# Kernel optimization log

Measured on AMD Instinct MI355X. Metric: run time of the kernel, lower is better.

The kernel has to match this reference:

```python
import jax, jax.numpy as jnp
import numpy as np

N_TOKENS = 16384
IN_FEATURES = 1024
OUT_FEATURES = 1024
BH = 32  # block rows (out dim)
BW = 32  # block cols (in dim)
N_BLOCKS = 256  # density 0.25 * (1024*1024/(32*32))


def setup_inputs() -> dict:
    key = jax.random.key(0)
    k1, k2, k3, k4 = jax.random.split(key, 4)
    x = jax.random.normal(k1, (N_TOKENS, IN_FEATURES), dtype=jnp.float32)
    weight_data = jax.random.normal(k2, (N_BLOCKS, BH, BW), dtype=jnp.float32)
    bias = jnp.zeros((OUT_FEATURES,), dtype=jnp.float32)
    block_row = jax.random.randint(k3, (N_BLOCKS,), 0, OUT_FEATURES // BH, dtype=jnp.int32)
    block_col = jax.random.randint(k4, (N_BLOCKS,), 0, IN_FEATURES // BW, dtype=jnp.int32)
    return {"x": x, "weight_data": weight_data, "bias": bias,
            "block_row": block_row, "block_col": block_col}


def reference(x, weight_data, bias, block_row, block_col):
    # Block-sparse linear: y = x @ W^T + bias, with W[out, in] stored as
    # N_BLOCKS dense (BH, BW) blocks at (block_row, block_col) block coords.
    N = x.shape[0]
    B, bh, bw = weight_data.shape
    n_row_blocks = bias.shape[0] // bh
    x3 = x.reshape(N, -1, bw)           # [N, in/bw, bw]
    xb = x3[:, block_col, :]            # gather input block-columns: [N, B, bw]
    # per-block partial output rows: data[b] @ x_colblock -> [N, B, bh]
    partial = jnp.einsum('nbw,bow->nbo', xb, weight_data)
    y3 = jnp.zeros((N, n_row_blocks, bh), dtype=x.dtype).at[:, block_row, :].add(partial)
    return y3.reshape(N, -1) + bias
```

## Files before the change

kernel.cpp:

```cpp
#include <hip/hip_runtime.h>

#define N_TOKENS 16384
#define IN_F 1024
#define OUT_F 1024
#define NB 256
#define BH 32
#define BW 32
#define NRB 32
#define T_TILE 32
#define NW 8
#define XS_STRIDE 1040
#define SCHED_ALLOC 304
#define WF_SLOT_SHORTS 1024
#define FLUSH_BIT (1 << 10)

#define WS_WF_BYTES   (SCHED_ALLOC * WF_SLOT_SHORTS * 2)
#define WS_SCHED_OFF  WS_WF_BYTES
#define WS_POS_OFF    (WS_SCHED_OFF + SCHED_ALLOC * 4)
#define WS_WSTART_OFF (WS_POS_OFF + NB * 4)

typedef short short8 __attribute__((ext_vector_type(8)));
typedef float float4v __attribute__((ext_vector_type(4)));

__device__ __forceinline__ short f2bf(float f) {
    unsigned u = __builtin_bit_cast(unsigned, f);
    u += 0x7fffu + ((u >> 16) & 1u);
    return (short)(u >> 16);
}

__global__ void prep_sched_kernel(const int* __restrict__ brow, const int* __restrict__ bcol,
                                  int* __restrict__ sched, int* __restrict__ pos_of,
                                  int* __restrict__ wstart, short* __restrict__ wf)
{
    __shared__ int cnt[NRB], start[NRB], cur[NRB];
    const int tid = threadIdx.x;
    if (tid < NRB) { cnt[tid] = 0; cur[tid] = 0; }
    __syncthreads();
    const int r = brow[tid];
    const int c = bcol[tid];
    atomicAdd(&cnt[r], 1);
    __syncthreads();
    if (tid < NRB) {
        const int w = tid & 7;
        int s = 0;
        for (int w2 = 0; w2 < w; ++w2) {
            int t = 0;
            for (int rr = w2; rr < NRB; rr += NW) t += (cnt[rr] ? cnt[rr] : 1);
            s += (t + 1) & ~1;
        }
        for (int rr = w; rr < tid; rr += NW) s += (cnt[rr] ? cnt[rr] : 1);
        start[tid] = s;
    }
    if (tid >= 64 && tid < 64 + NW + 1) {
        const int w = tid - 64;
        int s = 0;
        for (int w2 = 0; w2 < w; ++w2) {
            int t = 0;
            for (int rr = w2; rr < NRB; rr += NW) t += (cnt[rr] ? cnt[rr] : 1);
            s += (t + 1) & ~1;
        }
        wstart[w] = s;
    }
    if (tid >= 96 && tid < 96 + NW) {
        const int w = tid - 96;
        int base = 0;
        for (int w2 = 0; w2 < w; ++w2) {
            int t = 0;
            for (int rr = w2; rr < NRB; rr += NW) t += (cnt[rr] ? cnt[rr] : 1);
            base += (t + 1) & ~1;
        }
        int t = 0;
        for (int rr = w; rr < NRB; rr += NW) t += (cnt[rr] ? cnt[rr] : 1);
        if (t & 1) sched[base + t] = 0;
    }
    if (tid >= 128 && tid < 136) {
        int tot = 0;
        for (int w2 = 0; w2 < NW; ++w2) {
            int t = 0;
            for (int rr = w2; rr < NRB; rr += NW) t += (cnt[rr] ? cnt[rr] : 1);
            tot += (t + 1) & ~1;
        }
        sched[tot + (tid - 128)] = 0;
    }
    __syncthreads();
    const int slot = atomicAdd(&cur[r], 1);
    const int pos = start[r] + slot;
    sched[pos] = c | (r << 5) | ((slot == cnt[r] - 1) ? FLUSH_BIT : 0);
    pos_of[tid] = pos;
    if (tid < NRB && cnt[tid] == 0) {
        sched[start[tid]] = (tid << 5) | FLUSH_BIT;
        int4 z = {0, 0, 0, 0};
        int4* dst = (int4*)(wf + (size_t)start[tid] * WF_SLOT_SHORTS);
        for (int q = 0; q < WF_SLOT_SHORTS / 8; ++q) dst[q] = z;
    }
}

__global__ void prep_w_kernel(const float* __restrict__ wd, const int* __restrict__ pos_of,
                              short* __restrict__ wf)
{
    const int g = blockIdx.x * blockDim.x + threadIdx.x;
    const int lane = g & 63;
    const int oh = (g >> 6) & 1;
    const int b = g >> 7;
    const int l16 = lane & 15, quad = lane >> 4;
    const int pos = pos_of[b];
    const float* src = wd + (size_t)b * (BH * BW) + (oh * 16 + l16) * BW + quad * 8;
    const float4 w0 = *(const float4*)src;
    const float4 w1 = *(const float4*)(src + 4);
    short8 o;
    o[0] = f2bf(w0.x); o[1] = f2bf(w0.y); o[2] = f2bf(w0.z); o[3] = f2bf(w0.w);
    o[4] = f2bf(w1.x); o[5] = f2bf(w1.y); o[6] = f2bf(w1.z); o[7] = f2bf(w1.w);
    *(short8*)(wf + (size_t)pos * WF_SLOT_SHORTS + oh * 512 + lane * 8) = o;
}

__global__ __launch_bounds__(512, 4) void spmm_main_kernel(
    const float* __restrict__ x, const float* __restrict__ bias,
    const short* __restrict__ wf, const int* __restrict__ sched_g,
    const int* __restrict__ wstart_g, float* __restrict__ out)
{
    __shared__ short xs[T_TILE * XS_STRIDE];
    __shared__ int ssched[SCHED_ALLOC];
    __shared__ int swstart[NW + 1];

    const int tid = threadIdx.x;
    const int n0 = blockIdx.x * T_TILE;

    {
        const int tr = tid >> 7;
        const int tc = tid & 127;
        const float* xp = x + (size_t)(n0 + tr) * IN_F + tc * 8;
        short* sp = xs + tr * XS_STRIDE + tc * 8;
#pragma unroll
        for (int it = 0; it < T_TILE / 4; ++it) {
            const float4 a = *(const float4*)xp;
            const float4 b = *(const float4*)(xp + 4);
            short8 s;
            s[0] = f2bf(a.x); s[1] = f2bf(a.y); s[2] = f2bf(a.z); s[3] = f2bf(a.w);
            s[4] = f2bf(b.x); s[5] = f2bf(b.y); s[6] = f2bf(b.z); s[7] = f2bf(b.w);
            *(short8*)sp = s;
            xp += 4 * IN_F;
            sp += 4 * XS_STRIDE;
        }
    }
    if (tid < SCHED_ALLOC) ssched[tid] = sched_g[tid];
    if (tid < NW + 1) swstart[tid] = wstart_g[tid];
    __syncthreads();

    const int lane = tid & 63;
    const int wave = tid >> 6;
    const int l16 = lane & 15, quad = lane >> 4;

    const int s = swstart[wave];
    const int e = swstart[wave + 1];

    const short* x0 = xs + l16 * XS_STRIDE + quad * 8;
    const short* x1 = x0 + 16 * XS_STRIDE;
    const short* wfl = wf + lane * 8;

    int e0 = ssched[s], e1 = ssched[s + 1];
    int e2 = ssched[s + 2], e3 = ssched[s + 3];
    short8 cwA0 = *(const short8*)(wfl + (size_t)s * WF_SLOT_SHORTS);
    short8 cwB0 = *(const short8*)(wfl + (size_t)s * WF_SLOT_SHORTS + 512);
    short8 cwA1 = *(const short8*)(wfl + (size_t)(s + 1) * WF_SLOT_SHORTS);
    short8 cwB1 = *(const short8*)(wfl + (size_t)(s + 1) * WF_SLOT_SHORTS + 512);
    short8 nwA0 = *(const short8*)(wfl + (size_t)(s + 2) * WF_SLOT_SHORTS);
    short8 nwB0 = *(const short8*)(wfl + (size_t)(s + 2) * WF_SLOT_SHORTS + 512);
    short8 nwA1 = *(const short8*)(wfl + (size_t)(s + 3) * WF_SLOT_SHORTS);
    short8 nwB1 = *(const short8*)(wfl + (size_t)(s + 3) * WF_SLOT_SHORTS + 512);
    short8 a0t0 = *(const short8*)(x0 + (e0 & 31) * BW);
    short8 a0t1 = *(const short8*)(x1 + (e0 & 31) * BW);
    short8 a1t0 = *(const short8*)(x0 + (e1 & 31) * BW);
    short8 a1t1 = *(const short8*)(x1 + (e1 & 31) * BW);

    int rn = wave;
    float bv0 = bias[rn * BH + l16];
    float bv1 = bias[rn * BH + 16 + l16];

    float4v accA = {0.f, 0.f, 0.f, 0.f};
    float4v accB = {0.f, 0.f, 0.f, 0.f};
    float4v accC = {0.f, 0.f, 0.f, 0.f};
    float4v accD = {0.f, 0.f, 0.f, 0.f};

    auto flush = [&](int ev) {
        if (ev & FLUSH_BIT) {
            const int rr = (ev >> 5) & 31;
            const int ob = rr * BH + l16;
            float* op0 = out + (size_t)(n0 + quad * 4) * OUT_F + ob;
            float* op1 = op0 + (size_t)16 * OUT_F;
#pragma unroll
            for (int g = 0; g < 4; ++g) {
                op0[g * OUT_F]      = accA[g] + bv0;
                op0[g * OUT_F + 16] = accB[g] + bv1;
                op1[g * OUT_F]      = accC[g] + bv0;
                op1[g * OUT_F + 16] = accD[g] + bv1;
            }
            accA = (float4v){0.f, 0.f, 0.f, 0.f};
            accB = (float4v){0.f, 0.f, 0.f, 0.f};
            accC = (float4v){0.f, 0.f, 0.f, 0.f};
            accD = (float4v){0.f, 0.f, 0.f, 0.f};
            rn = (rn + NW) & 31;
            bv0 = bias[rn * BH + l16];
            bv1 = bias[rn * BH + 16 + l16];
        }
    };

    for (int k = s; k < e; k += 2) {
        const int e4 = ssched[k + 4];
        const int e5 = ssched[k + 5];
        const short8 fwA0 = *(const short8*)(wfl + (size_t)(k + 4) * WF_SLOT_SHORTS);
        const short8 fwB0 = *(const short8*)(wfl + (size_t)(k + 4) * WF_SLOT_SHORTS + 512);
        const short8 fwA1 = *(const short8*)(wfl + (size_t)(k + 5) * WF_SLOT_SHORTS);
        const short8 fwB1 = *(const short8*)(wfl + (size_t)(k + 5) * WF_SLOT_SHORTS + 512);
        const short8 na0t0 = *(const short8*)(x0 + (e2 & 31) * BW);
        const short8 na0t1 = *(const short8*)(x1 + (e2 & 31) * BW);
        const short8 na1t0 = *(const short8*)(x0 + (e3 & 31) * BW);
        const short8 na1t1 = *(const short8*)(x1 + (e3 & 31) * BW);

        accA = __builtin_amdgcn_mfma_f32_16x16x32_bf16(a0t0, cwA0, accA, 0, 0, 0);
        accB = __builtin_amdgcn_mfma_f32_16x16x32_bf16(a0t0, cwB0, accB, 0, 0, 0);
        accC = __builtin_amdgcn_mfma_f32_16x16x32_bf16(a0t1, cwA0, accC, 0, 0, 0);
        accD = __builtin_amdgcn_mfma_f32_16x16x32_bf16(a0t1, cwB0, accD, 0, 0, 0);
        flush(e0);
        accA = __builtin_amdgcn_mfma_f32_16x16x32_bf16(a1t0, cwA1, accA, 0, 0, 0);
        accB = __builtin_amdgcn_mfma_f32_16x16x32_bf16(a1t0, cwB1, accB, 0, 0, 0);
        accC = __builtin_amdgcn_mfma_f32_16x16x32_bf16(a1t1, cwA1, accC, 0, 0, 0);
        accD = __builtin_amdgcn_mfma_f32_16x16x32_bf16(a1t1, cwB1, accD, 0, 0, 0);
        flush(e1);

        e0 = e2; e1 = e3; e2 = e4; e3 = e5;
        a0t0 = na0t0; a0t1 = na0t1; a1t0 = na1t0; a1t1 = na1t1;
        cwA0 = nwA0; cwB0 = nwB0; cwA1 = nwA1; cwB1 = nwB1;
        nwA0 = fwA0; nwB0 = fwB0; nwA1 = fwA1; nwB1 = fwB1;
    }
}

extern "C" void kernel_launch(void* const* d_in, const int* in_sizes, int n_in,
                              void* d_out, int out_size, void* d_ws, size_t ws_size,
                              hipStream_t stream) {
    const float* x    = (const float*)d_in[0];
    const float* wd   = (const float*)d_in[1];
    const float* bias = (const float*)d_in[2];
    const int* brow   = (const int*)d_in[3];
    const int* bcol   = (const int*)d_in[4];
    float* out = (float*)d_out;

    char* ws = (char*)d_ws;
    short* wf   = (short*)ws;
    int* sched  = (int*)(ws + WS_SCHED_OFF);
    int* pos_of = (int*)(ws + WS_POS_OFF);
    int* wstart = (int*)(ws + WS_WSTART_OFF);

    prep_sched_kernel<<<1, 256, 0, stream>>>(brow, bcol, sched, pos_of, wstart, wf);
    prep_w_kernel<<<NB * 128 / 256, 256, 0, stream>>>(wd, pos_of, wf);
    spmm_main_kernel<<<N_TOKENS / T_TILE, 512, 0, stream>>>(x, bias, wf, sched, wstart, out);
}
```

Before: 134.8 us.

## Halve token tile, balance row-blocks across waves by load, cache bias in LDS

```diff
diff --git a/kernel.cpp b/kernel.cpp
--- a/kernel.cpp
+++ b/kernel.cpp
@@ -7,7 +7,7 @@
 #define BH 32
 #define BW 32
 #define NRB 32
-#define T_TILE 32
+#define T_TILE 16
 #define NW 8
 #define XS_STRIDE 1040
 #define SCHED_ALLOC 304
@@ -33,6 +33,8 @@
                                   int* __restrict__ wstart, short* __restrict__ wf)
 {
     __shared__ int cnt[NRB], start[NRB], cur[NRB];
+    __shared__ int eff[NRB], rnk[NRB], wv[NRB], off[NRB];
+    __shared__ int wtot[NW], pw[NW + 1];
     const int tid = threadIdx.x;
     if (tid < NRB) { cnt[tid] = 0; cur[tid] = 0; }
     __syncthreads();
@@ -40,48 +42,47 @@
     const int c = bcol[tid];
     atomicAdd(&cnt[r], 1);
     __syncthreads();
+    if (tid < NRB) eff[tid] = cnt[tid] ? cnt[tid] : 1;
+    __syncthreads();
     if (tid < NRB) {
-        const int w = tid & 7;
-        int s = 0;
-        for (int w2 = 0; w2 < w; ++w2) {
-            int t = 0;
-            for (int rr = w2; rr < NRB; rr += NW) t += (cnt[rr] ? cnt[rr] : 1);
-            s += (t + 1) & ~1;
+        const int e_ = eff[tid];
+        int rk = 0;
+        for (int j = 0; j < NRB; ++j) {
+            const int ej = eff[j];
+            if (ej > e_ || (ej == e_ && j < tid)) ++rk;
         }
-        for (int rr = w; rr < tid; rr += NW) s += (cnt[rr] ? cnt[rr] : 1);
-        start[tid] = s;
-    }
-    if (tid >= 64 && tid < 64 + NW + 1) {
-        const int w = tid - 64;
-        int s = 0;
-        for (int w2 = 0; w2 < w; ++w2) {
-            int t = 0;
-            for (int rr = w2; rr < NRB; rr += NW) t += (cnt[rr] ? cnt[rr] : 1);
-            s += (t + 1) & ~1;
-        }
-        wstart[w] = s;
-    }
-    if (tid >= 96 && tid < 96 + NW) {
-        const int w = tid - 96;
-        int base = 0;
-        for (int w2 = 0; w2 < w; ++w2) {
-            int t = 0;
-            for (int rr = w2; rr < NRB; rr += NW) t += (cnt[rr] ? cnt[rr] : 1);
-            base += (t + 1) & ~1;
-        }
+        rnk[tid] = rk;
+        const int s8 = rk & 7, dir = (rk >> 3) & 1;
+        wv[tid] = dir ? (7 - s8) : s8;
+    }
+    __syncthreads();
+    if (tid < NRB) {
+        const int w = wv[tid], rk = rnk[tid];
+        int o = 0;
+        for (int j = 0; j < NRB; ++j)
+            if (wv[j] == w && rnk[j] < rk) o += eff[j];
+        off[tid] = o;
+    }
+    if (tid >= NRB && tid < NRB + NW) {
+        const int w = tid - NRB;
         int t = 0;
-        for (int rr = w; rr < NRB; rr += NW) t += (cnt[rr] ? cnt[rr] : 1);
-        if (t & 1) sched[base + t] = 0;
-    }
-    if (tid >= 128 && tid < 136) {
-        int tot = 0;
-        for (int w2 = 0; w2 < NW; ++w2) {
-            int t = 0;
-            for (int rr = w2; rr < NRB; rr += NW) t += (cnt[rr] ? cnt[rr] : 1);
-            tot += (t + 1) & ~1;
-        }
-        sched[tot + (tid - 128)] = 0;
-    }
+        for (int j = 0; j < NRB; ++j) if (wv[j] == w) t += eff[j];
+        wtot[w] = t;
+    }
+    __syncthreads();
+    if (tid == 0) {
+        int ws = 0;
+        for (int w = 0; w < NW; ++w) { pw[w] = ws; ws += (wtot[w] + 1) & ~1; }
+        pw[NW] = ws;
+        for (int q = 0; q < 8; ++q) sched[ws + q] = 0;
+    }
+    __syncthreads();
+    if (tid < NRB) start[tid] = pw[wv[tid]] + off[tid];
+    if (tid < NW) {
+        wstart[tid] = pw[tid];
+        if (wtot[tid] & 1) sched[pw[tid] + wtot[tid]] = 0;
+    }
+    if (tid == NW) wstart[NW] = pw[NW];
     __syncthreads();
     const int slot = atomicAdd(&cur[r], 1);
     const int pos = start[r] + slot;
@@ -113,17 +114,34 @@
     *(short8*)(wf + (size_t)pos * WF_SLOT_SHORTS + oh * 512 + lane * 8) = o;
 }
 
-__global__ __launch_bounds__(512, 4) void spmm_main_kernel(
+__global__ __launch_bounds__(512, 8) void spmm_main_kernel(
     const float* __restrict__ x, const float* __restrict__ bias,
     const short* __restrict__ wf, const int* __restrict__ sched_g,
     const int* __restrict__ wstart_g, float* __restrict__ out)
 {
     __shared__ short xs[T_TILE * XS_STRIDE];
+    __shared__ float sbias[OUT_F];
     __shared__ int ssched[SCHED_ALLOC];
-    __shared__ int swstart[NW + 1];
 
     const int tid = threadIdx.x;
     const int n0 = blockIdx.x * T_TILE;
+    const int lane = tid & 63;
+    const int wave = tid >> 6;
+    const int l16 = lane & 15, quad = lane >> 4;
+
+    const int s = wstart_g[wave];
+    const int e = wstart_g[wave + 1];
+    int e0 = sched_g[s], e1 = sched_g[s + 1];
+    int e2 = sched_g[s + 2], e3 = sched_g[s + 3];
+    const short* wfl = wf + lane * 8;
+    short8 cwA0 = *(const short8*)(wfl + (size_t)s * WF_SLOT_SHORTS);
+    short8 cwB0 = *(const short8*)(wfl + (size_t)s * WF_SLOT_SHORTS + 512);
+    short8 cwA1 = *(const short8*)(wfl + (size_t)(s + 1) * WF_SLOT_SHORTS);
+    short8 cwB1 = *(const short8*)(wfl + (size_t)(s + 1) * WF_SLOT_SHORTS + 512);
+    short8 nwA0 = *(const short8*)(wfl + (size_t)(s + 2) * WF_SLOT_SHORTS);
+    short8 nwB0 = *(const short8*)(wfl + (size_t)(s + 2) * WF_SLOT_SHORTS + 512);
+    short8 nwA1 = *(const short8*)(wfl + (size_t)(s + 3) * WF_SLOT_SHORTS);
+    short8 nwB1 = *(const short8*)(wfl + (size_t)(s + 3) * WF_SLOT_SHORTS + 512);
 
     {
         const int tr = tid >> 7;
@@ -134,73 +152,40 @@
         for (int it = 0; it < T_TILE / 4; ++it) {
             const float4 a = *(const float4*)xp;
             const float4 b = *(const float4*)(xp + 4);
-            short8 s;
-            s[0] = f2bf(a.x); s[1] = f2bf(a.y); s[2] = f2bf(a.z); s[3] = f2bf(a.w);
-            s[4] = f2bf(b.x); s[5] = f2bf(b.y); s[6] = f2bf(b.z); s[7] = f2bf(b.w);
-            *(short8*)sp = s;
+            short8 sv;
+            sv[0] = f2bf(a.x); sv[1] = f2bf(a.y); sv[2] = f2bf(a.z); sv[3] = f2bf(a.w);
+            sv[4] = f2bf(b.x); sv[5] = f2bf(b.y); sv[6] = f2bf(b.z); sv[7] = f2bf(b.w);
+            *(short8*)sp = sv;
             xp += 4 * IN_F;
             sp += 4 * XS_STRIDE;
         }
     }
     if (tid < SCHED_ALLOC) ssched[tid] = sched_g[tid];
-    if (tid < NW + 1) swstart[tid] = wstart_g[tid];
-    __syncthreads();
-
-    const int lane = tid & 63;
-    const int wave = tid >> 6;
-    const int l16 = lane & 15, quad = lane >> 4;
-
-    const int s = swstart[wave];
-    const int e = swstart[wave + 1];
+    if (tid < OUT_F / 4) *(float4*)(sbias + tid * 4) = *(const float4*)(bias + tid * 4);
+    __syncthreads();
 
     const short* x0 = xs + l16 * XS_STRIDE + quad * 8;
-    const short* x1 = x0 + 16 * XS_STRIDE;
-    const short* wfl = wf + lane * 8;
-
-    int e0 = ssched[s], e1 = ssched[s + 1];
-    int e2 = ssched[s + 2], e3 = ssched[s + 3];
-    short8 cwA0 = *(const short8*)(wfl + (size_t)s * WF_SLOT_SHORTS);
-    short8 cwB0 = *(const short8*)(wfl + (size_t)s * WF_SLOT_SHORTS + 512);
-    short8 cwA1 = *(const short8*)(wfl + (size_t)(s + 1) * WF_SLOT_SHORTS);
-    short8 cwB1 = *(const short8*)(wfl + (size_t)(s + 1) * WF_SLOT_SHORTS + 512);
-    short8 nwA0 = *(const short8*)(wfl + (size_t)(s + 2) * WF_SLOT_SHORTS);
-    short8 nwB0 = *(const short8*)(wfl + (size_t)(s + 2) * WF_SLOT_SHORTS + 512);
-    short8 nwA1 = *(const short8*)(wfl + (size_t)(s + 3) * WF_SLOT_SHORTS);
-    short8 nwB1 = *(const short8*)(wfl + (size_t)(s + 3) * WF_SLOT_SHORTS + 512);
-    short8 a0t0 = *(const short8*)(x0 + (e0 & 31) * BW);
-    short8 a0t1 = *(const short8*)(x1 + (e0 & 31) * BW);
-    short8 a1t0 = *(const short8*)(x0 + (e1 & 31) * BW);
-    short8 a1t1 = *(const short8*)(x1 + (e1 & 31) * BW);
-
-    int rn = wave;
-    float bv0 = bias[rn * BH + l16];
-    float bv1 = bias[rn * BH + 16 + l16];
+    short8 a0 = *(const short8*)(x0 + (e0 & 31) * BW);
+    short8 a1 = *(const short8*)(x0 + (e1 & 31) * BW);
 
     float4v accA = {0.f, 0.f, 0.f, 0.f};
     float4v accB = {0.f, 0.f, 0.f, 0.f};
-    float4v accC = {0.f, 0.f, 0.f, 0.f};
-    float4v accD = {0.f, 0.f, 0.f, 0.f};
+    float* const outb = out + (size_t)(n0 + quad * 4) * OUT_F + l16;
 
     auto flush = [&](int ev) {
         if (ev & FLUSH_BIT) {
             const int rr = (ev >> 5) & 31;
-            const int ob = rr * BH + l16;
-            float* op0 = out + (size_t)(n0 + quad * 4) * OUT_F + ob;
-            float* op1 = op0 + (size_t)16 * OUT_F;
+            const int ob = rr * BH;
+            const float bv0 = sbias[ob + l16];
+            const float bv1 = sbias[ob + 16 + l16];
+            float* op = outb + ob;
 #pragma unroll
             for (int g = 0; g < 4; ++g) {
-                op0[g * OUT_F]      = accA[g] + bv0;
-                op0[g * OUT_F + 16] = accB[g] + bv1;
-                op1[g * OUT_F]      = accC[g] + bv0;
-                op1[g * OUT_F + 16] = accD[g] + bv1;
+                op[(size_t)g * OUT_F]      = accA[g] + bv0;
+                op[(size_t)g * OUT_F + 16] = accB[g] + bv1;
             }
             accA = (float4v){0.f, 0.f, 0.f, 0.f};
             accB = (float4v){0.f, 0.f, 0.f, 0.f};
-            accC = (float4v){0.f, 0.f, 0.f, 0.f};
-            accD = (float4v){0.f, 0.f, 0.f, 0.f};
-            rn = (rn + NW) & 31;
-            bv0 = bias[rn * BH + l16];
-            bv1 = bias[rn * BH + 16 + l16];
         }
     };
 
@@ -211,24 +196,18 @@
         const short8 fwB0 = *(const short8*)(wfl + (size_t)(k + 4) * WF_SLOT_SHORTS + 512);
         const short8 fwA1 = *(const short8*)(wfl + (size_t)(k + 5) * WF_SLOT_SHORTS);
         const short8 fwB1 = *(const short8*)(wfl + (size_t)(k + 5) * WF_SLOT_SHORTS + 512);
-        const short8 na0t0 = *(const short8*)(x0 + (e2 & 31) * BW);
-        const short8 na0t1 = *(const short8*)(x1 + (e2 & 31) * BW);
-        const short8 na1t0 = *(const short8*)(x0 + (e3 & 31) * BW);
-        const short8 na1t1 = *(const short8*)(x1 + (e3 & 31) * BW);
-
-        accA = __builtin_amdgcn_mfma_f32_16x16x32_bf16(a0t0, cwA0, accA, 0, 0, 0);
-        accB = __builtin_amdgcn_mfma_f32_16x16x32_bf16(a0t0, cwB0, accB, 0, 0, 0);
-        accC = __builtin_amdgcn_mfma_f32_16x16x32_bf16(a0t1, cwA0, accC, 0, 0, 0);
-        accD = __builtin_amdgcn_mfma_f32_16x16x32_bf16(a0t1, cwB0, accD, 0, 0, 0);
+        const short8 na0 = *(const short8*)(x0 + (e2 & 31) * BW);
+        const short8 na1 = *(const short8*)(x0 + (e3 & 31) * BW);
+
+        accA = __builtin_amdgcn_mfma_f32_16x16x32_bf16(a0, cwA0, accA, 0, 0, 0);
+        accB = __builtin_amdgcn_mfma_f32_16x16x32_bf16(a0, cwB0, accB, 0, 0, 0);
         flush(e0);
-        accA = __builtin_amdgcn_mfma_f32_16x16x32_bf16(a1t0, cwA1, accA, 0, 0, 0);
-        accB = __builtin_amdgcn_mfma_f32_16x16x32_bf16(a1t0, cwB1, accB, 0, 0, 0);
-        accC = __builtin_amdgcn_mfma_f32_16x16x32_bf16(a1t1, cwA1, accC, 0, 0, 0);
-        accD = __builtin_amdgcn_mfma_f32_16x16x32_bf16(a1t1, cwB1, accD, 0, 0, 0);
+        accA = __builtin_amdgcn_mfma_f32_16x16x32_bf16(a1, cwA1, accA, 0, 0, 0);
+        accB = __builtin_amdgcn_mfma_f32_16x16x32_bf16(a1, cwB1, accB, 0, 0, 0);
         flush(e1);
 
         e0 = e2; e1 = e3; e2 = e4; e3 = e5;
-        a0t0 = na0t0; a0t1 = na0t1; a1t0 = na1t0; a1t1 = na1t1;
+        a0 = na0; a1 = na1;
         cwA0 = nwA0; cwB0 = nwB0; cwA1 = nwA1; cwB1 = nwB1;
         nwA0 = fwA0; nwB0 = fwB0; nwA1 = fwA1; nwB1 = fwB1;
     }
```

Result: slower. 359.6 us (+166.8%).
